# Kernel optimization log

Measured on AMD Instinct MI355X. Metric: run time of the kernel, lower is better.

## Reference

```python
import jax, jax.numpy as jnp
import numpy as np

H = 512  # hidden_size

def _run_layer(xs, W_ih, W_hh, b_ih, b_hh):
    """xs: [T, B, D_in]. Returns (outputs [T,B,H], h_T [B,H], c_T [B,H])."""
    B = xs.shape[1]
    # Precompute input projections for all timesteps in one big GEMM.
    xg = jnp.einsum('tbd,gd->tbg', xs, W_ih) + b_ih + b_hh  # [T, B, 4H]
    W_hh_T = W_hh.T  # [H, 4H]
    h0 = jnp.zeros((B, H), xs.dtype)
    c0 = jnp.zeros((B, H), xs.dtype)

    def step(carry, xg_t):
        h, c = carry
        gates = xg_t + h @ W_hh_T  # [B, 4H]
        i_g, f_g, g_g, o_g = jnp.split(gates, 4, axis=1)
        i = jax.nn.sigmoid(i_g)
        f = jax.nn.sigmoid(f_g)
        g = jnp.tanh(g_g)
        o = jax.nn.sigmoid(o_g)
        c_next = f * c + i * g
        h_next = o * jnp.tanh(c_next)
        return (h_next, c_next), h_next

    (h_T, c_T), outs = jax.lax.scan(step, (h0, c0), xg)
    return outs, h_T, c_T


def setup_inputs() -> dict:
    key = jax.random.key(0)
    ks = jax.random.split(key, 9)
    B, T, D = 64, 2048, 512
    stdv = 1.0 / np.sqrt(H)
    u = lambda k, shape: jax.random.uniform(k, shape, jnp.float32, -stdv, stdv)
    return {
        'x': jax.random.normal(ks[0], (B, T, D), jnp.float32),
        'W_ih_0': u(ks[1], (4 * H, D)),
        'W_hh_0': u(ks[2], (4 * H, H)),
        'b_ih_0': u(ks[3], (4 * H,)),
        'b_hh_0': u(ks[4], (4 * H,)),
        'W_ih_1': u(ks[5], (4 * H, H)),
        'W_hh_1': u(ks[6], (4 * H, H)),
        'b_ih_1': u(ks[7], (4 * H,)),
        'b_hh_1': u(ks[8], (4 * H,)),
    }


def reference(x, W_ih_0, W_hh_0, b_ih_0, b_hh_0, W_ih_1, W_hh_1, b_ih_1, b_hh_1):
    # batch_first=True input [B, T, D] -> scan over time [T, B, D]
    xs = jnp.transpose(x, (1, 0, 2))
    out0, h0_T, c0_T = _run_layer(xs, W_ih_0, W_hh_0, b_ih_0, b_hh_0)
    out1, h1_T, c1_T = _run_layer(out0, W_ih_1, W_hh_1, b_ih_1, b_hh_1)
    output = jnp.transpose(out1, (1, 0, 2))  # [B, T, H]
    hn = jnp.stack([h0_T, h1_T], axis=0)  # [num_layers, B, H]
    cn = jnp.stack([c0_T, c1_T], axis=0)
    return output, hn, cn
```

## Files before the change

### kernel.cpp

```cpp
#include <hip/hip_runtime.h>
#include <hip/hip_bf16.h>

#define T_STEPS 2048
#define BATCH   64
#define HID     512
#define GATES   2048

typedef __attribute__((ext_vector_type(8))) short short8;
typedef __attribute__((ext_vector_type(4))) float f32x4;

__device__ inline unsigned short f2bf(float f) {
  union { float f; unsigned u; } v; v.f = f;
  unsigned r = v.u + 0x7fffu + ((v.u >> 16) & 1u);
  return (unsigned short)(r >> 16);
}
__device__ inline float bf2f(unsigned short s) {
  union { unsigned u; float f; } v; v.u = ((unsigned)s) << 16;
  return v.f;
}
__device__ inline float sigmoidf_(float x) { return 1.f / (1.f + __expf(-x)); }
__device__ inline float tanhf_(float x)    { return 2.f / (1.f + __expf(-2.f * x)) - 1.f; }

template<int ABF16, int TROWS>
__global__ __launch_bounds__(256) void proj_kernel(
    const void* __restrict__ Aptr, const float* __restrict__ W,
    const float* __restrict__ bias1, const float* __restrict__ bias2,
    unsigned short* __restrict__ out)
{
  __shared__ short As[128][72];
  __shared__ short Bs[128][72];
  const int tid  = threadIdx.x;
  const int lane = tid & 63;
  const int wv   = tid >> 6;
  const int wm   = wv >> 1, wn = wv & 1;
  const int bid  = blockIdx.x;
  const int nt   = bid & 15;
  const long mbase = (long)(bid >> 4) * 128;
  const int  nbase = nt * 128;

  f32x4 acc[4][4] = {};

  const int r  = tid >> 1;
  const int kh = (tid & 1) * 32;

  for (int kt = 0; kt < 8; ++kt) {
    if (ABF16) {
      const unsigned short* src = (const unsigned short*)Aptr + (mbase + r) * 512 + kt * 64 + kh;
      *(short8*)&As[r][kh]      = *(const short8*)(src);
      *(short8*)&As[r][kh + 8]  = *(const short8*)(src + 8);
      *(short8*)&As[r][kh + 16] = *(const short8*)(src + 16);
      *(short8*)&As[r][kh + 24] = *(const short8*)(src + 24);
    } else {
      const float* src = (const float*)Aptr + (mbase + r) * 512 + kt * 64 + kh;
#pragma unroll
      for (int j = 0; j < 4; ++j) {
        float4 v0 = *(const float4*)(src + j * 8);
        float4 v1 = *(const float4*)(src + j * 8 + 4);
        short8 p;
        p[0] = (short)f2bf(v0.x); p[1] = (short)f2bf(v0.y);
        p[2] = (short)f2bf(v0.z); p[3] = (short)f2bf(v0.w);
        p[4] = (short)f2bf(v1.x); p[5] = (short)f2bf(v1.y);
        p[6] = (short)f2bf(v1.z); p[7] = (short)f2bf(v1.w);
        *(short8*)&As[r][kh + j * 8] = p;
      }
    }
    {
      const float* src = W + (size_t)(nbase + r) * 512 + kt * 64 + kh;
#pragma unroll
      for (int j = 0; j < 4; ++j) {
        float4 v0 = *(const float4*)(src + j * 8);
        float4 v1 = *(const float4*)(src + j * 8 + 4);
        short8 p;
        p[0] = (short)f2bf(v0.x); p[1] = (short)f2bf(v0.y);
        p[2] = (short)f2bf(v0.z); p[3] = (short)f2bf(v0.w);
        p[4] = (short)f2bf(v1.x); p[5] = (short)f2bf(v1.y);
        p[6] = (short)f2bf(v1.z); p[7] = (short)f2bf(v1.w);
        *(short8*)&Bs[r][kh + j * 8] = p;
      }
    }
    __syncthreads();
#pragma unroll
    for (int kk = 0; kk < 2; ++kk) {
      const int kc = kk * 32 + ((lane >> 4) & 3) * 8;
      short8 af[4], bfr[4];
#pragma unroll
      for (int i = 0; i < 4; ++i)
        af[i] = *(const short8*)&As[wm * 64 + i * 16 + (lane & 15)][kc];
#pragma unroll
      for (int i = 0; i < 4; ++i)
        bfr[i] = *(const short8*)&Bs[wn * 64 + i * 16 + (lane & 15)][kc];
#pragma unroll
      for (int i = 0; i < 4; ++i)
#pragma unroll
        for (int j = 0; j < 4; ++j)
          acc[i][j] = __builtin_amdgcn_mfma_f32_16x16x32_bf16(af[i], bfr[j], acc[i][j], 0, 0, 0);
    }
    __syncthreads();
  }
#pragma unroll
  for (int j = 0; j < 4; ++j) {
    const int n = nbase + wn * 64 + j * 16 + (lane & 15);
    const float bsum = bias1[n] + bias2[n];
#pragma unroll
    for (int i = 0; i < 4; ++i) {
      f32x4 v = acc[i][j];
#pragma unroll
      for (int e = 0; e < 4; ++e) {
        long m = mbase + wm * 64 + i * 16 + ((lane >> 4) & 3) * 4 + e;
        long orow = TROWS ? ((m & 2047) * 64 + (m >> 11)) : m;
        out[orow * 2048 + n] = f2bf(v[e] + bsum);
      }
    }
  }
}

#define HLOAD16(PTR)                                                   \
      asm volatile(                                                    \
        "global_load_dwordx4 %0, %16, off sc0 sc1\n\t"                 \
        "global_load_dwordx4 %1, %16, off offset:64 sc0 sc1\n\t"       \
        "global_load_dwordx4 %2, %16, off offset:128 sc0 sc1\n\t"      \
        "global_load_dwordx4 %3, %16, off offset:192 sc0 sc1\n\t"      \
        "global_load_dwordx4 %4, %16, off offset:256 sc0 sc1\n\t"      \
        "global_load_dwordx4 %5, %16, off offset:320 sc0 sc1\n\t"      \
        "global_load_dwordx4 %6, %16, off offset:384 sc0 sc1\n\t"      \
        "global_load_dwordx4 %7, %16, off offset:448 sc0 sc1\n\t"      \
        "global_load_dwordx4 %8, %16, off offset:512 sc0 sc1\n\t"      \
        "global_load_dwordx4 %9, %16, off offset:576 sc0 sc1\n\t"      \
        "global_load_dwordx4 %10, %16, off offset:640 sc0 sc1\n\t"     \
        "global_load_dwordx4 %11, %16, off offset:704 sc0 sc1\n\t"     \
        "global_load_dwordx4 %12, %16, off offset:768 sc0 sc1\n\t"     \
        "global_load_dwordx4 %13, %16, off offset:832 sc0 sc1\n\t"     \
        "global_load_dwordx4 %14, %16, off offset:896 sc0 sc1\n\t"     \
        "global_load_dwordx4 %15, %16, off offset:960 sc0 sc1\n\t"     \
        "s_waitcnt vmcnt(8)"                                           \
        : "=&v"(hh[0]), "=&v"(hh[1]), "=&v"(hh[2]), "=&v"(hh[3]),      \
          "=&v"(hh[4]), "=&v"(hh[5]), "=&v"(hh[6]), "=&v"(hh[7]),      \
          "=&v"(hh[8]), "=&v"(hh[9]), "=&v"(hh[10]), "=&v"(hh[11]),    \
          "=&v"(hh[12]), "=&v"(hh[13]), "=&v"(hh[14]), "=&v"(hh[15])   \
        : "v"(PTR)                                                     \
        : "memory")

__device__ __forceinline__ void load_w_lds(const float* __restrict__ Whh,
                                           int u_base, int tid, char* smem) {
  const int r    = tid >> 1;
  const int kh   = (tid & 1) * 256;
  const int type = r >> 5, uu = r & 31;
  const float* src = Whh + (size_t)(type * 512 + u_base + uu) * 512 + kh;
  const int rowbyte = r * 1024;
  const int sw = (r & 7) << 4;
#pragma unroll 4
  for (int j = 0; j < 32; ++j) {
    float4 v0 = *(const float4*)(src + j * 8);
    float4 v1 = *(const float4*)(src + j * 8 + 4);
    short8 p;
    p[0] = (short)f2bf(v0.x); p[1] = (short)f2bf(v0.y);
    p[2] = (short)f2bf(v0.z); p[3] = (short)f2bf(v0.w);
    p[4] = (short)f2bf(v1.x); p[5] = (short)f2bf(v1.y);
    p[6] = (short)f2bf(v1.z); p[7] = (short)f2bf(v1.w);
    int byte = rowbyte + (kh + j * 8) * 2;
    *(short8*)(smem + (byte ^ sw)) = p;
  }
}

__device__ void scan0_role(
    int bid0, const unsigned short* __restrict__ xg, const float* __restrict__ Whh,
    unsigned short* __restrict__ hhist, float* __restrict__ dout,
    int* __restrict__ flags, char* smem)
{
  float* gbuf = (float*)(smem + 131072);
  float* cbuf = (float*)(smem + 131072 + 16 * 132 * 4);
  const int tid  = threadIdx.x;
  const int lane = tid & 63;
  const int wv   = tid >> 6;
  const int s    = bid0 & 15;
  const int grp  = bid0 >> 4;
  const int u_base = s * 32;
  const int b_base = grp * 16;
  int* gflags = flags + grp * (16 * 32);

  load_w_lds(Whh, u_base, tid, smem);
  cbuf[tid] = 0.f; cbuf[tid + 256] = 0.f;
  __syncthreads();

  const int bb = tid >> 4;
  const int u0 = (tid & 15) * 2;
  const int rowA = wv * 32 + (lane & 15);
  const int rowB = rowA + 16;
  const int kb   = ((lane >> 4) & 3) * 16;
  const int swA  = (rowA & 7) << 4;
  const int swB  = (rowB & 7) << 4;

  for (int t = 0; t < T_STEPS; ++t) {
    unsigned xgp[4];
    {
      const size_t base = ((size_t)t * 64 + b_base + bb) * 2048 + u_base + u0;
      xgp[0] = *(const unsigned*)(xg + base);
      xgp[1] = *(const unsigned*)(xg + base + 512);
      xgp[2] = *(const unsigned*)(xg + base + 1024);
      xgp[3] = *(const unsigned*)(xg + base + 1536);
    }

    f32x4 a0a = {0.f, 0.f, 0.f, 0.f}, a1a = {0.f, 0.f, 0.f, 0.f};
    f32x4 a0b = {0.f, 0.f, 0.f, 0.f}, a1b = {0.f, 0.f, 0.f, 0.f};

    if (t > 0) {
      {
        int f;
        do {
          f = __hip_atomic_load(&gflags[(lane & 15) * 32], __ATOMIC_RELAXED, __HIP_MEMORY_SCOPE_AGENT);
        } while (!__all(f >= t));
      }
      const unsigned short* hrow = hhist + (size_t)t * (64 * 512)
          + (size_t)(b_base + (lane & 15)) * 512 + ((lane >> 4) & 3) * 8;
      short8 hh[16];
      HLOAD16(hrow);
      __builtin_amdgcn_sched_barrier(0);

#pragma unroll
      for (int kt = 0; kt < 8; ++kt) {
        short8 b0 = *(const short8*)(smem + ((rowA * 1024 + kt * 64 + kb) ^ swA));
        short8 b1 = *(const short8*)(smem + ((rowB * 1024 + kt * 64 + kb) ^ swB));
        a0a = __builtin_amdgcn_mfma_f32_16x16x32_bf16(hh[kt], b0, a0a, 0, 0, 0);
        a1a = __builtin_amdgcn_mfma_f32_16x16x32_bf16(hh[kt], b1, a1a, 0, 0, 0);
      }
      asm volatile("s_waitcnt vmcnt(0)" ::: "memory");
      __builtin_amdgcn_sched_barrier(0);
#pragma unroll
      for (int kt = 8; kt < 16; ++kt) {
        short8 b0 = *(const short8*)(smem + ((rowA * 1024 + kt * 64 + kb) ^ swA));
        short8 b1 = *(const short8*)(smem + ((rowB * 1024 + kt * 64 + kb) ^ swB));
        a0b = __builtin_amdgcn_mfma_f32_16x16x32_bf16(hh[kt], b0, a0b, 0, 0, 0);
        a1b = __builtin_amdgcn_mfma_f32_16x16x32_bf16(hh[kt], b1, a1b, 0, 0, 0);
      }
    }

    {
      const int m0 = ((lane >> 4) & 3) * 4;
      const int cA = wv * 32 + (lane & 15);
#pragma unroll
      for (int e = 0; e < 4; ++e) {
        gbuf[(m0 + e) * 132 + cA]      = a0a[e] + a0b[e];
        gbuf[(m0 + e) * 132 + cA + 16] = a1a[e] + a1b[e];
      }
    }
    __syncthreads();

    float hv[2], cv[2];
#pragma unroll
    for (int q = 0; q < 2; ++q) {
      const int u = u0 + q;
      float ig = gbuf[bb * 132 + u]        + bf2f((unsigned short)(xgp[0] >> (16 * q)));
      float fg = gbuf[bb * 132 + 32 + u]   + bf2f((unsigned short)(xgp[1] >> (16 * q)));
      float gg = gbuf[bb * 132 + 64 + u]   + bf2f((unsigned short)(xgp[2] >> (16 * q)));
      float og = gbuf[bb * 132 + 96 + u]   + bf2f((unsigned short)(xgp[3] >> (16 * q)));
      float iv = sigmoidf_(ig), fv = sigmoidf_(fg);
      float gv = tanhf_(gg),    ov = sigmoidf_(og);
      float c = fv * cbuf[bb * 32 + u] + iv * gv;
      cbuf[bb * 32 + u] = c;
      float h = ov * tanhf_(c);
      hv[q] = h; cv[q] = c;
    }
    {
      unsigned hp = (unsigned)f2bf(hv[0]) | ((unsigned)f2bf(hv[1]) << 16);
      __hip_atomic_store(
          (unsigned*)(hhist + (size_t)(t + 1) * (64 * 512) + (size_t)(b_base + bb) * 512 + u_base + u0),
          hp, __ATOMIC_RELAXED, __HIP_MEMORY_SCOPE_AGENT);
      if (t == T_STEPS - 1) {
        const size_t OUT0 = (size_t)64 * 2048 * 512;
        size_t o  = OUT0 + (size_t)(b_base + bb) * 512 + u_base + u0;
        dout[o]     = hv[0];
        dout[o + 1] = hv[1];
        size_t oc = o + 65536;
        dout[oc]     = cv[0];
        dout[oc + 1] = cv[1];
      }
    }
    __syncthreads();
    if (tid == 0)
      __hip_atomic_store(&gflags[s * 32], t + 1, __ATOMIC_RELAXED, __HIP_MEMORY_SCOPE_AGENT);
  }
}

__device__ void scan1_role(
    int bid0, const float* __restrict__ Whh1, const float* __restrict__ Wih1,
    const float* __restrict__ bih1, const float* __restrict__ bhh1,
    const unsigned short* __restrict__ h0hist, unsigned short* __restrict__ h1hist,
    float* __restrict__ dout, const int* __restrict__ flg0, int* __restrict__ flg1,
    char* smem)
{
  float* gbuf = (float*)(smem + 131072);
  float* cbuf = (float*)(smem + 131072 + 16 * 132 * 4);
  const int tid  = threadIdx.x;
  const int lane = tid & 63;
  const int wv   = tid >> 6;
  const int s    = bid0 & 15;
  const int grp  = bid0 >> 4;
  const int u_base = s * 32;
  const int b_base = grp * 16;

  load_w_lds(Whh1, u_base, tid, smem);
  cbuf[tid] = 0.f; cbuf[tid + 256] = 0.f;
  __syncthreads();

  const int bb = tid >> 4;
  const int u0 = (tid & 15) * 2;
  const int rowA = wv * 32 + (lane & 15);
  const int rowB = rowA + 16;
  const int kb   = ((lane >> 4) & 3) * 16;
  const int swA  = (rowA & 7) << 4;
  const int swB  = (rowB & 7) << 4;

  short8 wib0[16], wib1[16];
  {
    const int k0 = ((lane >> 4) & 3) * 8;
    const int growA = (rowA >> 5) * 512 + u_base + (rowA & 31);
    const int growB = (rowB >> 5) * 512 + u_base + (rowB & 31);
#pragma unroll
    for (int kt = 0; kt < 16; ++kt) {
      const float* sA = Wih1 + (size_t)growA * 512 + kt * 32 + k0;
      const float* sB = Wih1 + (size_t)growB * 512 + kt * 32 + k0;
      short8 pa, pb;
#pragma unroll
      for (int e = 0; e < 8; ++e) { pa[e] = (short)f2bf(sA[e]); pb[e] = (short)f2bf(sB[e]); }
      wib0[kt] = pa; wib1[kt] = pb;
    }
  }
  float bias_[4][2];
#pragma unroll
  for (int ty = 0; ty < 4; ++ty)
#pragma unroll
    for (int q = 0; q < 2; ++q)
      bias_[ty][q] = bih1[ty * 512 + u_base + u0 + q] + bhh1[ty * 512 + u_base + u0 + q];

  const int pl = lane & 31;
  const int* pollp = (pl < 16) ? (flg1 + (grp * 16 + pl) * 32)
                               : (flg0 + (grp * 16 + (pl - 16)) * 32);
  const int thr_add = (pl < 16) ? 0 : 1;
  int* flp = flg1 + (grp * 16 + s) * 32;

  for (int t = 0; t < T_STEPS; ++t) {
    {
      int f;
      do {
        f = __hip_atomic_load(pollp, __ATOMIC_RELAXED, __HIP_MEMORY_SCOPE_AGENT);
      } while (!__all(f >= t + thr_add));
    }

    f32x4 a0a = {0.f, 0.f, 0.f, 0.f}, a1a = {0.f, 0.f, 0.f, 0.f};
    f32x4 a0b = {0.f, 0.f, 0.f, 0.f}, a1b = {0.f, 0.f, 0.f, 0.f};
    short8 hh[16];

    if (t > 0) {
      const unsigned short* hr1 = h1hist + (size_t)t * (64 * 512)
          + (size_t)(b_base + (lane & 15)) * 512 + ((lane >> 4) & 3) * 8;
      HLOAD16(hr1);
      __builtin_amdgcn_sched_barrier(0);
#pragma unroll
      for (int kt = 0; kt < 8; ++kt) {
        short8 b0 = *(const short8*)(smem + ((rowA * 1024 + kt * 64 + kb) ^ swA));
        short8 b1 = *(const short8*)(smem + ((rowB * 1024 + kt * 64 + kb) ^ swB));
        a0a = __builtin_amdgcn_mfma_f32_16x16x32_bf16(hh[kt], b0, a0a, 0, 0, 0);
        a1a = __builtin_amdgcn_mfma_f32_16x16x32_bf16(hh[kt], b1, a1a, 0, 0, 0);
      }
      asm volatile("s_waitcnt vmcnt(0)" ::: "memory");
      __builtin_amdgcn_sched_barrier(0);
#pragma unroll
      for (int kt = 8; kt < 16; ++kt) {
        short8 b0 = *(const short8*)(smem + ((rowA * 1024 + kt * 64 + kb) ^ swA));
        short8 b1 = *(const short8*)(smem + ((rowB * 1024 + kt * 64 + kb) ^ swB));
        a0b = __builtin_amdgcn_mfma_f32_16x16x32_bf16(hh[kt], b0, a0b, 0, 0, 0);
        a1b = __builtin_amdgcn_mfma_f32_16x16x32_bf16(hh[kt], b1, a1b, 0, 0, 0);
      }
    }
    {
      const unsigned short* hr0 = h0hist + (size_t)(t + 1) * (64 * 512)
          + (size_t)(b_base + (lane & 15)) * 512 + ((lane >> 4) & 3) * 8;
      HLOAD16(hr0);
      __builtin_amdgcn_sched_barrier(0);
#pragma unroll
      for (int kt = 0; kt < 8; ++kt) {
        a0a = __builtin_amdgcn_mfma_f32_16x16x32_bf16(hh[kt], wib0[kt], a0a, 0, 0, 0);
        a1a = __builtin_amdgcn_mfma_f32_16x16x32_bf16(hh[kt], wib1[kt], a1a, 0, 0, 0);
      }
      asm volatile("s_waitcnt vmcnt(0)" ::: "memory");
      __builtin_amdgcn_sched_barrier(0);
#pragma unroll
      for (int kt = 8; kt < 16; ++kt) {
        a0b = __builtin_amdgcn_mfma_f32_16x16x32_bf16(hh[kt], wib0[kt], a0b, 0, 0, 0);
        a1b = __builtin_amdgcn_mfma_f32_16x16x32_bf16(hh[kt], wib1[kt], a1b, 0, 0, 0);
      }
    }

    {
      const int m0 = ((lane >> 4) & 3) * 4;
      const int cA = wv * 32 + (lane & 15);
#pragma unroll
      for (int e = 0; e < 4; ++e) {
        gbuf[(m0 + e) * 132 + cA]      = a0a[e] + a0b[e];
        gbuf[(m0 + e) * 132 + cA + 16] = a1a[e] + a1b[e];
      }
    }
    __syncthreads();

    float hv[2], cv[2];
#pragma unroll
    for (int q = 0; q < 2; ++q) {
      const int u = u0 + q;
      float ig = gbuf[bb * 132 + u]        + bias_[0][q];
      float fg = gbuf[bb * 132 + 32 + u]   + bias_[1][q];
      float gg = gbuf[bb * 132 + 64 + u]   + bias_[2][q];
      float og = gbuf[bb * 132 + 96 + u]   + bias_[3][q];
      float iv = sigmoidf_(ig), fv = sigmoidf_(fg);
      float gv = tanhf_(gg),    ov = sigmoidf_(og);
      float c = fv * cbuf[bb * 32 + u] + iv * gv;
      cbuf[bb * 32 + u] = c;
      float h = ov * tanhf_(c);
      hv[q] = h; cv[q] = c;
    }
    {
      unsigned hp = (unsigned)f2bf(hv[0]) | ((unsigned)f2bf(hv[1]) << 16);
      __hip_atomic_store(
          (unsigned*)(h1hist + (size_t)(t + 1) * (64 * 512) + (size_t)(b_base + bb) * 512 + u_base + u0),
          hp, __ATOMIC_RELAXED, __HIP_MEMORY_SCOPE_AGENT);
      float2 ho; ho.x = hv[0]; ho.y = hv[1];
      *(float2*)(dout + (size_t)(b_base + bb) * ((size_t)T_STEPS * 512) + (size_t)t * 512 + u_base + u0) = ho;
      if (t == T_STEPS - 1) {
        const size_t OUT0 = (size_t)64 * 2048 * 512;
        size_t o  = OUT0 + 32768 + (size_t)(b_base + bb) * 512 + u_base + u0;
        dout[o]     = hv[0];
        dout[o + 1] = hv[1];
        size_t oc = o + 65536;
        dout[oc]     = cv[0];
        dout[oc + 1] = cv[1];
      }
    }
    __syncthreads();
    if (tid == 0)
      __hip_atomic_store(flp, t + 1, __ATOMIC_RELAXED, __HIP_MEMORY_SCOPE_AGENT);
  }
}

__global__ __launch_bounds__(256, 1) void scan_fused(
    const unsigned short* __restrict__ xg,
    const float* __restrict__ Whh0, const float* __restrict__ Whh1,
    const float* __restrict__ Wih1, const float* __restrict__ bih1,
    const float* __restrict__ bhh1,
    unsigned short* __restrict__ h0hist, unsigned short* __restrict__ h1hist,
    float* __restrict__ dout,
    int* __restrict__ flg0, int* __restrict__ flg1)
{
  extern __shared__ char smem[];
  const int bid = blockIdx.x;
  if (bid < 64)
    scan0_role(bid, xg, Whh0, h0hist, dout, flg0, smem);
  else
    scan1_role(bid - 64, Whh1, Wih1, bih1, bhh1, h0hist, h1hist, dout, flg0, flg1, smem);
}

extern "C" void kernel_launch(void* const* d_in, const int* in_sizes, int n_in,
                              void* d_out, int out_size, void* d_ws, size_t ws_size,
                              hipStream_t stream) {
  const float* x    = (const float*)d_in[0];
  const float* Wih0 = (const float*)d_in[1];
  const float* Whh0 = (const float*)d_in[2];
  const float* bih0 = (const float*)d_in[3];
  const float* bhh0 = (const float*)d_in[4];
  const float* Wih1 = (const float*)d_in[5];
  const float* Whh1 = (const float*)d_in[6];
  const float* bih1 = (const float*)d_in[7];
  const float* bhh1 = (const float*)d_in[8];
  float* out = (float*)d_out;

  const size_t XG_BYTES   = (size_t)T_STEPS * 64 * 2048 * 2;
  const size_t H_BYTES    = (size_t)(T_STEPS + 1) * 64 * 512 * 2;
  const size_t FLAG_BYTES = (size_t)2 * 4 * 16 * 32 * 4;
  if (ws_size < XG_BYTES + 2 * H_BYTES + FLAG_BYTES) return;

  char* ws = (char*)d_ws;
  unsigned short* xg = (unsigned short*)ws;
  unsigned short* h0 = (unsigned short*)(ws + XG_BYTES);
  unsigned short* h1 = (unsigned short*)(ws + XG_BYTES + H_BYTES);
  int* flags         = (int*)(ws + XG_BYTES + 2 * H_BYTES);
  int* flg0 = flags;
  int* flg1 = flags + 4 * 16 * 32;

  hipMemsetAsync(flags, 0, FLAG_BYTES, stream);

  const int smem_scan = 131072 + 16 * 132 * 4 + 2048;
  hipFuncSetAttribute((const void*)scan_fused, hipFuncAttributeMaxDynamicSharedMemorySize, smem_scan);

  proj_kernel<0, 1><<<dim3(16384), dim3(256), 0, stream>>>(x, Wih0, bih0, bhh0, xg);
  scan_fused<<<dim3(128), dim3(256), smem_scan, stream>>>(
      xg, Whh0, Whh1, Wih1, bih1, bhh1, h0, h1, out, flg0, flg1);
}
```

Baseline: 12.44 ms.

## Prefetch layer-0 hidden state ahead of layer-1 flag wait and reorder MFMAs

In the layer-1 recurrent loop, the layer-0 output h0[t+1] is now loaded before spinning on the layer-1 readiness flags. The layer-0 flag requirement is relaxed to run two steps ahead, so that load is off the critical path. The input-projection MFMAs run first, while the h1 history load is still in flight, which hides recurrent-load latency behind compute. This costs 16 extra short8 registers and a stricter dependency on layer 0 staying ahead, which could add pressure or waiting.

```diff
diff --git a/kernel.cpp b/kernel.cpp
--- a/kernel.cpp
+++ b/kernel.cpp
@@ -114,7 +114,7 @@
   }
 }
 
-#define HLOAD16(PTR)                                                   \
+#define HLOAD16W(ARR, PTR)                                             \
       asm volatile(                                                    \
         "global_load_dwordx4 %0, %16, off sc0 sc1\n\t"                 \
         "global_load_dwordx4 %1, %16, off offset:64 sc0 sc1\n\t"       \
@@ -133,10 +133,35 @@
         "global_load_dwordx4 %14, %16, off offset:896 sc0 sc1\n\t"     \
         "global_load_dwordx4 %15, %16, off offset:960 sc0 sc1\n\t"     \
         "s_waitcnt vmcnt(8)"                                           \
-        : "=&v"(hh[0]), "=&v"(hh[1]), "=&v"(hh[2]), "=&v"(hh[3]),      \
-          "=&v"(hh[4]), "=&v"(hh[5]), "=&v"(hh[6]), "=&v"(hh[7]),      \
-          "=&v"(hh[8]), "=&v"(hh[9]), "=&v"(hh[10]), "=&v"(hh[11]),    \
-          "=&v"(hh[12]), "=&v"(hh[13]), "=&v"(hh[14]), "=&v"(hh[15])   \
+        : "=&v"(ARR[0]), "=&v"(ARR[1]), "=&v"(ARR[2]), "=&v"(ARR[3]),  \
+          "=&v"(ARR[4]), "=&v"(ARR[5]), "=&v"(ARR[6]), "=&v"(ARR[7]),  \
+          "=&v"(ARR[8]), "=&v"(ARR[9]), "=&v"(ARR[10]), "=&v"(ARR[11]),\
+          "=&v"(ARR[12]), "=&v"(ARR[13]), "=&v"(ARR[14]), "=&v"(ARR[15])\
+        : "v"(PTR)                                                     \
+        : "memory")
+
+#define HLOAD16I(ARR, PTR)                                             \
+      asm volatile(                                                    \
+        "global_load_dwordx4 %0, %16, off sc0 sc1\n\t"                 \
+        "global_load_dwordx4 %1, %16, off offset:64 sc0 sc1\n\t"       \
+        "global_load_dwordx4 %2, %16, off offset:128 sc0 sc1\n\t"      \
+        "global_load_dwordx4 %3, %16, off offset:192 sc0 sc1\n\t"      \
+        "global_load_dwordx4 %4, %16, off offset:256 sc0 sc1\n\t"      \
+        "global_load_dwordx4 %5, %16, off offset:320 sc0 sc1\n\t"      \
+        "global_load_dwordx4 %6, %16, off offset:384 sc0 sc1\n\t"      \
+        "global_load_dwordx4 %7, %16, off offset:448 sc0 sc1\n\t"      \
+        "global_load_dwordx4 %8, %16, off offset:512 sc0 sc1\n\t"      \
+        "global_load_dwordx4 %9, %16, off offset:576 sc0 sc1\n\t"      \
+        "global_load_dwordx4 %10, %16, off offset:640 sc0 sc1\n\t"     \
+        "global_load_dwordx4 %11, %16, off offset:704 sc0 sc1\n\t"     \
+        "global_load_dwordx4 %12, %16, off offset:768 sc0 sc1\n\t"     \
+        "global_load_dwordx4 %13, %16, off offset:832 sc0 sc1\n\t"     \
+        "global_load_dwordx4 %14, %16, off offset:896 sc0 sc1\n\t"     \
+        "global_load_dwordx4 %15, %16, off offset:960 sc0 sc1"         \
+        : "=&v"(ARR[0]), "=&v"(ARR[1]), "=&v"(ARR[2]), "=&v"(ARR[3]),  \
+          "=&v"(ARR[4]), "=&v"(ARR[5]), "=&v"(ARR[6]), "=&v"(ARR[7]),  \
+          "=&v"(ARR[8]), "=&v"(ARR[9]), "=&v"(ARR[10]), "=&v"(ARR[11]),\
+          "=&v"(ARR[12]), "=&v"(ARR[13]), "=&v"(ARR[14]), "=&v"(ARR[15])\
         : "v"(PTR)                                                     \
         : "memory")
 
@@ -213,7 +238,7 @@
       const unsigned short* hrow = hhist + (size_t)t * (64 * 512)
           + (size_t)(b_base + (lane & 15)) * 512 + ((lane >> 4) & 3) * 8;
       short8 hh[16];
-      HLOAD16(hrow);
+      HLOAD16W(hh, hrow);
       __builtin_amdgcn_sched_barrier(0);
 
 #pragma unroll
@@ -335,16 +360,32 @@
   const int pl = lane & 31;
   const int* pollp = (pl < 16) ? (flg1 + (grp * 16 + pl) * 32)
                                : (flg0 + (grp * 16 + (pl - 16)) * 32);
-  const int thr_add = (pl < 16) ? 0 : 1;
+  const int* p0 = flg0 + (grp * 16 + (lane & 15)) * 32;
   int* flp = flg1 + (grp * 16 + s) * 32;
 
+  {
+    int f;
+    do {
+      f = __hip_atomic_load(p0, __ATOMIC_RELAXED, __HIP_MEMORY_SCOPE_AGENT);
+    } while (!__all(f >= 1));
+  }
+
   for (int t = 0; t < T_STEPS; ++t) {
-    {
+    short8 gg[16];
+    {
+      const unsigned short* hr0 = h0hist + (size_t)(t + 1) * (64 * 512)
+          + (size_t)(b_base + (lane & 15)) * 512 + ((lane >> 4) & 3) * 8;
+      HLOAD16I(gg, hr0);
+    }
+    {
+      const int need = (pl < 16) ? t : ((t + 2 < T_STEPS) ? t + 2 : T_STEPS);
       int f;
       do {
         f = __hip_atomic_load(pollp, __ATOMIC_RELAXED, __HIP_MEMORY_SCOPE_AGENT);
-      } while (!__all(f >= t + thr_add));
-    }
+      } while (!__all(f >= need));
+    }
+    asm volatile("s_waitcnt vmcnt(0)" ::: "memory");
+    __builtin_amdgcn_sched_barrier(0);
 
     f32x4 a0a = {0.f, 0.f, 0.f, 0.f}, a1a = {0.f, 0.f, 0.f, 0.f};
     f32x4 a0b = {0.f, 0.f, 0.f, 0.f}, a1b = {0.f, 0.f, 0.f, 0.f};
@@ -353,7 +394,23 @@
     if (t > 0) {
       const unsigned short* hr1 = h1hist + (size_t)t * (64 * 512)
           + (size_t)(b_base + (lane & 15)) * 512 + ((lane >> 4) & 3) * 8;
-      HLOAD16(hr1);
+      HLOAD16I(hh, hr1);
+      __builtin_amdgcn_sched_barrier(0);
+    }
+
+#pragma unroll
+    for (int kt = 0; kt < 8; ++kt) {
+      a0a = __builtin_amdgcn_mfma_f32_16x16x32_bf16(gg[kt], wib0[kt], a0a, 0, 0, 0);
+      a1a = __builtin_amdgcn_mfma_f32_16x16x32_bf16(gg[kt], wib1[kt], a1a, 0, 0, 0);
+    }
+#pragma unroll
+    for (int kt = 8; kt < 16; ++kt) {
+      a0b = __builtin_amdgcn_mfma_f32_16x16x32_bf16(gg[kt], wib0[kt], a0b, 0, 0, 0);
+      a1b = __builtin_amdgcn_mfma_f32_16x16x32_bf16(gg[kt], wib1[kt], a1b, 0, 0, 0);
+    }
+
+    if (t > 0) {
+      asm volatile("s_waitcnt vmcnt(8)" ::: "memory");
       __builtin_amdgcn_sched_barrier(0);
 #pragma unroll
       for (int kt = 0; kt < 8; ++kt) {
@@ -372,24 +429,6 @@
         a1b = __builtin_amdgcn_mfma_f32_16x16x32_bf16(hh[kt], b1, a1b, 0, 0, 0);
       }
     }
-    {
-      const unsigned short* hr0 = h0hist + (size_t)(t + 1) * (64 * 512)
-          + (size_t)(b_base + (lane & 15)) * 512 + ((lane >> 4) & 3) * 8;
-      HLOAD16(hr0);
-      __builtin_amdgcn_sched_barrier(0);
-#pragma unroll
-      for (int kt = 0; kt < 8; ++kt) {
-        a0a = __builtin_amdgcn_mfma_f32_16x16x32_bf16(hh[kt], wib0[kt], a0a, 0, 0, 0);
-        a1a = __builtin_amdgcn_mfma_f32_16x16x32_bf16(hh[kt], wib1[kt], a1a, 0, 0, 0);
-      }
-      asm volatile("s_waitcnt vmcnt(0)" ::: "memory");
-      __builtin_amdgcn_sched_barrier(0);
-#pragma unroll
-      for (int kt = 8; kt < 16; ++kt) {
-        a0b = __builtin_amdgcn_mfma_f32_16x16x32_bf16(hh[kt], wib0[kt], a0b, 0, 0, 0);
-        a1b = __builtin_amdgcn_mfma_f32_16x16x32_bf16(hh[kt], wib1[kt], a1b, 0, 0, 0);
-      }
-    }
 
     {
       const int m0 = ((lane >> 4) & 3) * 4;
@@ -408,10 +447,10 @@
       const int u = u0 + q;
       float ig = gbuf[bb * 132 + u]        + bias_[0][q];
       float fg = gbuf[bb * 132 + 32 + u]   + bias_[1][q];
-      float gg = gbuf[bb * 132 + 64 + u]   + bias_[2][q];
+      float gg2 = gbuf[bb * 132 + 64 + u]  + bias_[2][q];
       float og = gbuf[bb * 132 + 96 + u]   + bias_[3][q];
       float iv = sigmoidf_(ig), fv = sigmoidf_(fg);
-      float gv = tanhf_(gg),    ov = sigmoidf_(og);
+      float gv = tanhf_(gg2),   ov = sigmoidf_(og);
       float c = fv * cbuf[bb * 32 + u] + iv * gv;
       cbuf[bb * 32 + u] = c;
       float h = ov * tanhf_(c);
```

Result: no change. 12.38 ms (-0.5%).
